# Kernel optimization log

Hardware: AMD Instinct MI355X
Metric: run time of the kernel (lower is better)

The kernel has to match this reference:

```python
import jax, jax.numpy as jnp
import numpy as np

EPS = 1e-12

def _l2norm(v, axis):
    return v / jnp.maximum(jnp.linalg.norm(v, axis=axis, keepdims=True), EPS)

def setup_inputs() -> dict:
    key = jax.random.key(0)
    k1, k2, k3 = jax.random.split(key, 3)
    B, D, C = 65536, 768, 100
    P = C * (C - 1) // 2  # 4950 pairwise local heads
    x = jax.random.normal(k1, (B, D), dtype=jnp.float32)
    first_out = jax.random.normal(k2, (B, C), dtype=jnp.float32)
    weights = jax.random.normal(k3, (P, 2, D), dtype=jnp.float32) * (1.0 / np.sqrt(D))
    sigma = jnp.ones((P,), dtype=jnp.float32)
    return {"x": x, "first_out": first_out, "weights": weights, "sigma": sigma, "cur_stage": 4}

def reference(x, first_out, weights, sigma, cur_stage):
    # top-2 class indices per sample, sorted ascending -> pair key (a, b), a < b
    _, top2 = jax.lax.top_k(first_out, 2)              # [B, 2]
    sorted_idx = jnp.sort(top2, axis=1)                # [B, 2]
    a = sorted_idx[:, 0]
    b = sorted_idx[:, 1]
    pair_idx = b * (b - 1) // 2 + a                    # key 'a-b' -> flat head index
    W = weights[pair_idx]                              # [B, 2, D] gathered expert weights
    s = sigma[pair_idx]                                # [B]
    # CosineLinear (use_RP=False): sigma * normalize(x) @ normalize(W)^T
    xn = _l2norm(x, axis=1)                            # [B, D]
    Wn = _l2norm(W, axis=2)                            # [B, 2, D]
    logits = s[:, None] * jnp.einsum('bd,bkd->bk', xn, Wn)  # [B, 2]
    # pick which of the two candidate classes the local head prefers
    sel = jnp.argmax(logits, axis=1)                   # [B]
    preds = jnp.take_along_axis(sorted_idx, sel[:, None], axis=1)[:, 0]  # [B]
    return preds, logits
```

## Files before the change

### kernel.cpp

```cpp
#include <hip/hip_runtime.h>
#include <math.h>


#define D_DIM 768
#define C_DIM 100
#define F4_PER_ROW (D_DIM / 4)
#define EPS_N 1e-12f

__device__ __forceinline__ bool vi_gt(float v0, int i0, float v1, int i1) {
    return (v0 > v1) || (v0 == v1 && i0 < i1);
}

__global__ __launch_bounds__(256) void mlcl_kernel(
    const float* __restrict__ x,
    const float* __restrict__ first_out,
    const float* __restrict__ weights,
    const float* __restrict__ sigma,
    float* __restrict__ out,
    int B)
{
    const int lane = threadIdx.x & 63;
    const int wave = threadIdx.x >> 6;
    const int r = blockIdx.x * 4 + wave;
    if (r >= B) return;

    const float* fo = first_out + (size_t)r * C_DIM;
    float e0 = fo[lane];
    int   j1 = lane + 64;
    float e1 = (j1 < C_DIM) ? fo[j1] : -INFINITY;

    float v1, v2; int i1, i2;
    if (vi_gt(e1, j1, e0, lane)) { v1 = e1; i1 = j1;  v2 = e0; i2 = lane; }
    else                         { v1 = e0; i1 = lane; v2 = e1; i2 = j1; }

    #pragma unroll
    for (int m = 1; m < 64; m <<= 1) {
        float ov1 = __shfl_xor(v1, m, 64);
        int   oi1 = __shfl_xor(i1, m, 64);
        float ov2 = __shfl_xor(v2, m, 64);
        int   oi2 = __shfl_xor(i2, m, 64);
        if (vi_gt(ov1, oi1, v1, i1)) {
            float nv2; int ni2;
            if (vi_gt(v1, i1, ov2, oi2)) { nv2 = v1;  ni2 = i1; }
            else                         { nv2 = ov2; ni2 = oi2; }
            v1 = ov1; i1 = oi1; v2 = nv2; i2 = ni2;
        } else {
            if (vi_gt(ov1, oi1, v2, i2)) { v2 = ov1; i2 = oi1; }
        }
    }
    const int a = min(i1, i2);
    const int b = max(i1, i2);
    const int pair = b * (b - 1) / 2 + a;

    const float4* xv = (const float4*)(x + (size_t)r * D_DIM);
    const float4* w0 = (const float4*)(weights + (size_t)pair * (2 * D_DIM));
    const float4* w1 = w0 + F4_PER_ROW;

    double xx = 0.0, d0 = 0.0, d1 = 0.0, n0 = 0.0, n1 = 0.0;
    #pragma unroll
    for (int j = 0; j < 3; ++j) {
        const int idx = lane + j * 64;
        float4 xa = xv[idx];
        float4 wa = w0[idx];
        float4 wb = w1[idx];
        xx += (double)xa.x * xa.x + (double)xa.y * xa.y + (double)xa.z * xa.z + (double)xa.w * xa.w;
        d0 += (double)xa.x * wa.x + (double)xa.y * wa.y + (double)xa.z * wa.z + (double)xa.w * wa.w;
        d1 += (double)xa.x * wb.x + (double)xa.y * wb.y + (double)xa.z * wb.z + (double)xa.w * wb.w;
        n0 += (double)wa.x * wa.x + (double)wa.y * wa.y + (double)wa.z * wa.z + (double)wa.w * wa.w;
        n1 += (double)wb.x * wb.x + (double)wb.y * wb.y + (double)wb.z * wb.z + (double)wb.w * wb.w;
    }
    #pragma unroll
    for (int m = 1; m < 64; m <<= 1) {
        xx += __shfl_xor(xx, m, 64);
        d0 += __shfl_xor(d0, m, 64);
        d1 += __shfl_xor(d1, m, 64);
        n0 += __shfl_xor(n0, m, 64);
        n1 += __shfl_xor(n1, m, 64);
    }

    if (lane == 0) {
        double s   = (double)sigma[pair];
        double inx = 1.0 / fmax(sqrt(xx), (double)EPS_N);
        double l0  = s * d0 * inx / fmax(sqrt(n0), (double)EPS_N);
        double l1  = s * d1 * inx / fmax(sqrt(n1), (double)EPS_N);
        int sel = (l1 > l0) ? 1 : 0;
        out[r] = (float)(sel ? b : a);
        out[B + 2 * r]     = (float)l0;
        out[B + 2 * r + 1] = (float)l1;
    }
}

extern "C" void kernel_launch(void* const* d_in, const int* in_sizes, int n_in,
                              void* d_out, int out_size, void* d_ws, size_t ws_size,
                              hipStream_t stream) {
    const float* x         = (const float*)d_in[0];
    const float* first_out = (const float*)d_in[1];
    const float* weights   = (const float*)d_in[2];
    const float* sigma     = (const float*)d_in[3];
    float* out = (float*)d_out;

    const int B = in_sizes[0] / D_DIM;
    dim3 grid((B + 3) / 4), block(256);
    hipLaunchKernelGGL(mlcl_kernel, grid, block, 0, stream,
                       x, first_out, weights, sigma, out, B);
}
```

Measured before the change: 336.0 us.

## Precompute per-head weight inverse norms and split top-2 into separate kernel

Adds a kernel that computes the inverse L2 norm of each of the 9900 weight rows once, instead of recomputing both norms for every sample. The top-2 selection moves into its own kernel that writes packed (a,b) indices to workspace, and the main kernel reads them. The x self-norm is accumulated in float instead of double, which cuts FP64 work but may introduce small rounding differences. The cost is two extra launches plus a workspace round trip for the indices.

```diff
diff --git a/kernel.cpp b/kernel.cpp
--- a/kernel.cpp
+++ b/kernel.cpp
@@ -4,24 +4,43 @@
 
 #define D_DIM 768
 #define C_DIM 100
+#define P_DIM 4950
 #define F4_PER_ROW (D_DIM / 4)
-#define EPS_N 1e-12f
+#define EPS_N 1e-12
 
 __device__ __forceinline__ bool vi_gt(float v0, int i0, float v1, int i1) {
     return (v0 > v1) || (v0 == v1 && i0 < i1);
 }
 
-__global__ __launch_bounds__(256) void mlcl_kernel(
-    const float* __restrict__ x,
+__global__ __launch_bounds__(256) void norm_kernel(
+    const float* __restrict__ weights,
+    double* __restrict__ invn,
+    int nrows)
+{
+    const int lane = threadIdx.x & 63;
+    const int row = (blockIdx.x << 2) + (threadIdx.x >> 6);
+    if (row >= nrows) return;
+
+    const float4* wv = (const float4*)(weights + (size_t)row * D_DIM);
+    double n = 0.0;
+    #pragma unroll
+    for (int j = 0; j < 3; ++j) {
+        float4 w = wv[lane + j * 64];
+        n += (double)w.x * w.x + (double)w.y * w.y
+           + (double)w.z * w.z + (double)w.w * w.w;
+    }
+    #pragma unroll
+    for (int m = 1; m < 64; m <<= 1) n += __shfl_xor(n, m, 64);
+    if (lane == 0) invn[row] = 1.0 / fmax(sqrt(n), EPS_N);
+}
+
+__global__ __launch_bounds__(256) void top2_kernel(
     const float* __restrict__ first_out,
-    const float* __restrict__ weights,
-    const float* __restrict__ sigma,
-    float* __restrict__ out,
+    int* __restrict__ abbuf,
     int B)
 {
     const int lane = threadIdx.x & 63;
-    const int wave = threadIdx.x >> 6;
-    const int r = blockIdx.x * 4 + wave;
+    const int r = (blockIdx.x << 2) + (threadIdx.x >> 6);
     if (r >= B) return;
 
     const float* fo = first_out + (size_t)r * C_DIM;
@@ -30,7 +49,7 @@
     float e1 = (j1 < C_DIM) ? fo[j1] : -INFINITY;
 
     float v1, v2; int i1, i2;
-    if (vi_gt(e1, j1, e0, lane)) { v1 = e1; i1 = j1;  v2 = e0; i2 = lane; }
+    if (vi_gt(e1, j1, e0, lane)) { v1 = e1; i1 = j1;   v2 = e0; i2 = lane; }
     else                         { v1 = e0; i1 = lane; v2 = e1; i2 = j1; }
 
     #pragma unroll
@@ -48,41 +67,61 @@
             if (vi_gt(ov1, oi1, v2, i2)) { v2 = ov1; i2 = oi1; }
         }
     }
-    const int a = min(i1, i2);
-    const int b = max(i1, i2);
+    if (lane == 0) {
+        const int a = min(i1, i2);
+        const int b = max(i1, i2);
+        abbuf[r] = a | (b << 16);
+    }
+}
+
+__global__ __launch_bounds__(256) void main_kernel(
+    const float* __restrict__ x,
+    const float* __restrict__ weights,
+    const float* __restrict__ sigma,
+    const double* __restrict__ invn,
+    const int* __restrict__ abbuf,
+    float* __restrict__ out,
+    int B)
+{
+    const int lane = threadIdx.x & 63;
+    const int r = (blockIdx.x << 2) + (threadIdx.x >> 6);
+    if (r >= B) return;
+
+    const int ab = abbuf[r];
+    const int a = ab & 0xffff;
+    const int b = ab >> 16;
     const int pair = b * (b - 1) / 2 + a;
 
     const float4* xv = (const float4*)(x + (size_t)r * D_DIM);
     const float4* w0 = (const float4*)(weights + (size_t)pair * (2 * D_DIM));
     const float4* w1 = w0 + F4_PER_ROW;
 
-    double xx = 0.0, d0 = 0.0, d1 = 0.0, n0 = 0.0, n1 = 0.0;
+    float  xx = 0.0f;
+    double d0 = 0.0, d1 = 0.0;
     #pragma unroll
     for (int j = 0; j < 3; ++j) {
         const int idx = lane + j * 64;
         float4 xa = xv[idx];
         float4 wa = w0[idx];
         float4 wb = w1[idx];
-        xx += (double)xa.x * xa.x + (double)xa.y * xa.y + (double)xa.z * xa.z + (double)xa.w * xa.w;
-        d0 += (double)xa.x * wa.x + (double)xa.y * wa.y + (double)xa.z * wa.z + (double)xa.w * wa.w;
-        d1 += (double)xa.x * wb.x + (double)xa.y * wb.y + (double)xa.z * wb.z + (double)xa.w * wb.w;
-        n0 += (double)wa.x * wa.x + (double)wa.y * wa.y + (double)wa.z * wa.z + (double)wa.w * wa.w;
-        n1 += (double)wb.x * wb.x + (double)wb.y * wb.y + (double)wb.z * wb.z + (double)wb.w * wb.w;
+        xx += xa.x * xa.x + xa.y * xa.y + xa.z * xa.z + xa.w * xa.w;
+        d0 += (double)xa.x * wa.x + (double)xa.y * wa.y
+            + (double)xa.z * wa.z + (double)xa.w * wa.w;
+        d1 += (double)xa.x * wb.x + (double)xa.y * wb.y
+            + (double)xa.z * wb.z + (double)xa.w * wb.w;
     }
     #pragma unroll
     for (int m = 1; m < 64; m <<= 1) {
         xx += __shfl_xor(xx, m, 64);
         d0 += __shfl_xor(d0, m, 64);
         d1 += __shfl_xor(d1, m, 64);
-        n0 += __shfl_xor(n0, m, 64);
-        n1 += __shfl_xor(n1, m, 64);
     }
 
     if (lane == 0) {
-        double s   = (double)sigma[pair];
-        double inx = 1.0 / fmax(sqrt(xx), (double)EPS_N);
-        double l0  = s * d0 * inx / fmax(sqrt(n0), (double)EPS_N);
-        double l1  = s * d1 * inx / fmax(sqrt(n1), (double)EPS_N);
+        double s    = (double)sigma[pair];
+        double sinx = s / fmax(sqrt((double)xx), EPS_N);
+        double l0   = sinx * d0 * invn[2 * pair];
+        double l1   = sinx * d1 * invn[2 * pair + 1];
         int sel = (l1 > l0) ? 1 : 0;
         out[r] = (float)(sel ? b : a);
         out[B + 2 * r]     = (float)l0;
@@ -100,7 +139,15 @@
     float* out = (float*)d_out;
 
     const int B = in_sizes[0] / D_DIM;
-    dim3 grid((B + 3) / 4), block(256);
-    hipLaunchKernelGGL(mlcl_kernel, grid, block, 0, stream,
-                       x, first_out, weights, sigma, out, B);
+    const int NW = 2 * P_DIM;
+
+    double* invn = (double*)d_ws;
+    int* abbuf   = (int*)((char*)d_ws + (size_t)NW * sizeof(double));
+
+    hipLaunchKernelGGL(norm_kernel, dim3((NW + 3) / 4), dim3(256), 0, stream,
+                       weights, invn, NW);
+    hipLaunchKernelGGL(top2_kernel, dim3((B + 3) / 4), dim3(256), 0, stream,
+                       first_out, abbuf, B);
+    hipLaunchKernelGGL(main_kernel, dim3((B + 3) / 4), dim3(256), 0, stream,
+                       x, weights, sigma, invn, abbuf, out, B);
 }
```

Result: no change. 335.7 us (-0.1%).

## Bucket rows by expert pair to reuse gathered weights and precomputed norms

Applied to the files above, without the earlier changes.

Splits the kernel into a top-2 pass that records pair ids and counts, a prefix scan, a scatter building per-pair row lists, and a per-pair kernel. Each pair block loads its two weight rows into registers once and computes their norms once, then processes the rows assigned to that pair, two at a time per wave. This removes the repeated per-row weight gathers and norm computations, at the cost of extra launches, atomics, a serial single-block scan and uneven work per block.

```diff
diff --git a/kernel.cpp b/kernel.cpp
--- a/kernel.cpp
+++ b/kernel.cpp
@@ -4,24 +4,29 @@
 
 #define D_DIM 768
 #define C_DIM 100
-#define F4_PER_ROW (D_DIM / 4)
-#define EPS_N 1e-12f
+#define P_DIM 4950
+#define F4_ROW (D_DIM / 4)
+#define EPS_N 1e-12
+
+typedef float vf4 __attribute__((ext_vector_type(4)));
 
 __device__ __forceinline__ bool vi_gt(float v0, int i0, float v1, int i1) {
     return (v0 > v1) || (v0 == v1 && i0 < i1);
 }
 
-__global__ __launch_bounds__(256) void mlcl_kernel(
-    const float* __restrict__ x,
+#define DOT4D(acc, u, v) \
+    acc += (double)u.x * v.x + (double)u.y * v.y + (double)u.z * v.z + (double)u.w * v.w
+#define SQ4F(acc, u) \
+    acc += u.x * u.x + u.y * u.y + u.z * u.z + u.w * u.w
+
+__global__ __launch_bounds__(256) void top2_kernel(
     const float* __restrict__ first_out,
-    const float* __restrict__ weights,
-    const float* __restrict__ sigma,
-    float* __restrict__ out,
+    int* __restrict__ pairbuf,
+    int* __restrict__ counts,
     int B)
 {
     const int lane = threadIdx.x & 63;
-    const int wave = threadIdx.x >> 6;
-    const int r = blockIdx.x * 4 + wave;
+    const int r = (blockIdx.x << 2) + (threadIdx.x >> 6);
     if (r >= B) return;
 
     const float* fo = first_out + (size_t)r * C_DIM;
@@ -30,7 +35,7 @@
     float e1 = (j1 < C_DIM) ? fo[j1] : -INFINITY;
 
     float v1, v2; int i1, i2;
-    if (vi_gt(e1, j1, e0, lane)) { v1 = e1; i1 = j1;  v2 = e0; i2 = lane; }
+    if (vi_gt(e1, j1, e0, lane)) { v1 = e1; i1 = j1;   v2 = e0; i2 = lane; }
     else                         { v1 = e0; i1 = lane; v2 = e1; i2 = j1; }
 
     #pragma unroll
@@ -48,45 +53,147 @@
             if (vi_gt(ov1, oi1, v2, i2)) { v2 = ov1; i2 = oi1; }
         }
     }
-    const int a = min(i1, i2);
-    const int b = max(i1, i2);
-    const int pair = b * (b - 1) / 2 + a;
-
-    const float4* xv = (const float4*)(x + (size_t)r * D_DIM);
-    const float4* w0 = (const float4*)(weights + (size_t)pair * (2 * D_DIM));
-    const float4* w1 = w0 + F4_PER_ROW;
-
-    double xx = 0.0, d0 = 0.0, d1 = 0.0, n0 = 0.0, n1 = 0.0;
+    if (lane == 0) {
+        const int a = min(i1, i2);
+        const int b = max(i1, i2);
+        const int p = b * (b - 1) / 2 + a;
+        pairbuf[r] = p;
+        atomicAdd(&counts[p], 1);
+    }
+}
+
+#define SCAN_T 256
+#define CHUNK ((P_DIM + SCAN_T - 1) / SCAN_T)
+__global__ __launch_bounds__(SCAN_T) void scan_kernel(
+    const int* __restrict__ counts,
+    int* __restrict__ offsets)
+{
+    __shared__ int sh[SCAN_T];
+    const int t = threadIdx.x;
+    int vals[CHUNK];
+    int tot = 0;
+    #pragma unroll
+    for (int j = 0; j < CHUNK; ++j) {
+        const int idx = t * CHUNK + j;
+        const int v = (idx < P_DIM) ? counts[idx] : 0;
+        vals[j] = v; tot += v;
+    }
+    sh[t] = tot;
+    __syncthreads();
+    for (int d = 1; d < SCAN_T; d <<= 1) {
+        const int v = (t >= d) ? sh[t - d] : 0;
+        __syncthreads();
+        sh[t] += v;
+        __syncthreads();
+    }
+    int run = (t == 0) ? 0 : sh[t - 1];
+    #pragma unroll
+    for (int j = 0; j < CHUNK; ++j) {
+        const int idx = t * CHUNK + j;
+        if (idx < P_DIM) offsets[idx] = run;
+        run += vals[j];
+    }
+}
+
+__global__ __launch_bounds__(256) void scatter_kernel(
+    const int* __restrict__ pairbuf,
+    const int* __restrict__ offsets,
+    int* __restrict__ cursors,
+    int* __restrict__ rowlist,
+    int B)
+{
+    const int r = blockIdx.x * 256 + threadIdx.x;
+    if (r >= B) return;
+    const int p = pairbuf[r];
+    const int pos = offsets[p] + atomicAdd(&cursors[p], 1);
+    rowlist[pos] = r;
+}
+
+__global__ __launch_bounds__(256) void pair_kernel(
+    const float* __restrict__ x,
+    const float* __restrict__ weights,
+    const float* __restrict__ sigma,
+    const int* __restrict__ counts,
+    const int* __restrict__ offsets,
+    const int* __restrict__ rowlist,
+    float* __restrict__ out,
+    int B)
+{
+    const int p = blockIdx.x;
+    const int cnt = counts[p];
+    if (cnt == 0) return;
+    const int base = offsets[p];
+    const int lane = threadIdx.x & 63;
+    const int wave = threadIdx.x >> 6;
+
+    int b = (int)floor((sqrt(8.0 * (double)p + 1.0) + 1.0) * 0.5);
+    if (b * (b - 1) / 2 > p) --b;
+    if ((b + 1) * b / 2 <= p) ++b;
+    const int a = p - b * (b - 1) / 2;
+
+    const vf4* wv = (const vf4*)(weights + (size_t)p * (2 * D_DIM));
+    vf4 w0[3], w1[3];
+    double n0 = 0.0, n1 = 0.0;
     #pragma unroll
     for (int j = 0; j < 3; ++j) {
-        const int idx = lane + j * 64;
-        float4 xa = xv[idx];
-        float4 wa = w0[idx];
-        float4 wb = w1[idx];
-        xx += (double)xa.x * xa.x + (double)xa.y * xa.y + (double)xa.z * xa.z + (double)xa.w * xa.w;
-        d0 += (double)xa.x * wa.x + (double)xa.y * wa.y + (double)xa.z * wa.z + (double)xa.w * wa.w;
-        d1 += (double)xa.x * wb.x + (double)xa.y * wb.y + (double)xa.z * wb.z + (double)xa.w * wb.w;
-        n0 += (double)wa.x * wa.x + (double)wa.y * wa.y + (double)wa.z * wa.z + (double)wa.w * wa.w;
-        n1 += (double)wb.x * wb.x + (double)wb.y * wb.y + (double)wb.z * wb.z + (double)wb.w * wb.w;
+        w0[j] = wv[lane + j * 64];
+        w1[j] = wv[F4_ROW + lane + j * 64];
+        DOT4D(n0, w0[j], w0[j]);
+        DOT4D(n1, w1[j], w1[j]);
     }
     #pragma unroll
     for (int m = 1; m < 64; m <<= 1) {
-        xx += __shfl_xor(xx, m, 64);
-        d0 += __shfl_xor(d0, m, 64);
-        d1 += __shfl_xor(d1, m, 64);
         n0 += __shfl_xor(n0, m, 64);
         n1 += __shfl_xor(n1, m, 64);
     }
-
-    if (lane == 0) {
-        double s   = (double)sigma[pair];
-        double inx = 1.0 / fmax(sqrt(xx), (double)EPS_N);
-        double l0  = s * d0 * inx / fmax(sqrt(n0), (double)EPS_N);
-        double l1  = s * d1 * inx / fmax(sqrt(n1), (double)EPS_N);
-        int sel = (l1 > l0) ? 1 : 0;
-        out[r] = (float)(sel ? b : a);
-        out[B + 2 * r]     = (float)l0;
-        out[B + 2 * r + 1] = (float)l1;
+    const double s    = (double)sigma[p];
+    const double si0  = s / fmax(sqrt(n0), EPS_N);
+    const double si1  = s / fmax(sqrt(n1), EPS_N);
+
+    for (int i = wave * 2; i < cnt; i += 8) {
+        const int r0 = rowlist[base + i];
+        const bool has2 = (i + 1 < cnt);
+        const int r1 = has2 ? rowlist[base + i + 1] : r0;
+
+        const vf4* xa = (const vf4*)(x + (size_t)r0 * D_DIM);
+        const vf4* xb = (const vf4*)(x + (size_t)r1 * D_DIM);
+
+        float  xx0 = 0.f, xx1 = 0.f;
+        double d00 = 0.0, d01 = 0.0, d10 = 0.0, d11 = 0.0;
+        #pragma unroll
+        for (int j = 0; j < 3; ++j) {
+            const vf4 va = xa[lane + j * 64];
+            const vf4 vb = xb[lane + j * 64];
+            SQ4F(xx0, va);
+            SQ4F(xx1, vb);
+            DOT4D(d00, va, w0[j]);
+            DOT4D(d01, va, w1[j]);
+            DOT4D(d10, vb, w0[j]);
+            DOT4D(d11, vb, w1[j]);
+        }
+        #pragma unroll
+        for (int m = 1; m < 64; m <<= 1) {
+            xx0 += __shfl_xor(xx0, m, 64);
+            xx1 += __shfl_xor(xx1, m, 64);
+            d00 += __shfl_xor(d00, m, 64);
+            d01 += __shfl_xor(d01, m, 64);
+            d10 += __shfl_xor(d10, m, 64);
+            d11 += __shfl_xor(d11, m, 64);
+        }
+
+        if (lane == 0 || (lane == 1 && has2)) {
+            const int    rr  = lane ? r1 : r0;
+            const float  xxv = lane ? xx1 : xx0;
+            const double dd0 = lane ? d10 : d00;
+            const double dd1 = lane ? d11 : d01;
+            const double inx = 1.0 / fmax(sqrt((double)xxv), EPS_N);
+            const double l0  = si0 * dd0 * inx;
+            const double l1  = si1 * dd1 * inx;
+            const int sel = (l1 > l0) ? 1 : 0;
+            out[rr] = (float)(sel ? b : a);
+            out[B + 2 * rr]     = (float)l0;
+            out[B + 2 * rr + 1] = (float)l1;
+        }
     }
 }
 
@@ -100,7 +207,21 @@
     float* out = (float*)d_out;
 
     const int B = in_sizes[0] / D_DIM;
-    dim3 grid((B + 3) / 4), block(256);
-    hipLaunchKernelGGL(mlcl_kernel, grid, block, 0, stream,
-                       x, first_out, weights, sigma, out, B);
-}
+    const int P = in_sizes[3];
+
+    int* counts  = (int*)d_ws;
+    int* cursors = counts + P;
+    int* offsets = cursors + P;
+    int* pairbuf = offsets + P;
+    int* rowlist = pairbuf + B;
+
+    hipMemsetAsync(counts, 0, 2 * (size_t)P * sizeof(int), stream);
+    hipLaunchKernelGGL(top2_kernel, dim3((B + 3) / 4), dim3(256), 0, stream,
+                       first_out, pairbuf, counts, B);
+    hipLaunchKernelGGL(scan_kernel, dim3(1), dim3(SCAN_T), 0, stream,
+                       counts, offsets);
+    hipLaunchKernelGGL(scatter_kernel, dim3((B + 255) / 256), dim3(256), 0, stream,
+                       pairbuf, offsets, cursors, rowlist, B);
+    hipLaunchKernelGGL(pair_kernel, dim3(P), dim3(256), 0, stream,
+                       x, weights, sigma, counts, offsets, rowlist, out, B);
+}
```

Result: slower. 363.9 us (+8.3%).

## Assign four threads per row instead of a full wavefront per row

Applied to the files above, without the earlier changes.

Each output row is now handled by a group of 4 lanes rather than a whole 64-lane wavefront. Every lane runs a serial top-2 scan over its slice of first_out and accumulates the dot products over 48 float4 steps, so the cross-lane shuffle reductions shrink from 6 stages to 2. The x squared-norm accumulator also drops from double to float, and the two logits are written with a single float2 store. The intent is to cut shuffle and reduction overhead and the idle lanes, at the cost of strided, less coalesced float4 loads per lane and a longer serial loop per thread.

```diff
diff --git a/kernel.cpp b/kernel.cpp
--- a/kernel.cpp
+++ b/kernel.cpp
@@ -4,14 +4,21 @@
 
 #define D_DIM 768
 #define C_DIM 100
-#define F4_PER_ROW (D_DIM / 4)
-#define EPS_N 1e-12f
+#define EPS_N 1e-12
+
+typedef float vf4 __attribute__((ext_vector_type(4)));
 
 __device__ __forceinline__ bool vi_gt(float v0, int i0, float v1, int i1) {
     return (v0 > v1) || (v0 == v1 && i0 < i1);
 }
 
-__global__ __launch_bounds__(256) void mlcl_kernel(
+__device__ __forceinline__ void t2up(float val, int idx,
+                                     float& v1, int& i1, float& v2, int& i2) {
+    if (vi_gt(val, idx, v1, i1)) { v2 = v1; i2 = i1; v1 = val; i1 = idx; }
+    else if (vi_gt(val, idx, v2, i2)) { v2 = val; i2 = idx; }
+}
+
+__global__ __launch_bounds__(256) void fused_kernel(
     const float* __restrict__ x,
     const float* __restrict__ first_out,
     const float* __restrict__ weights,
@@ -19,22 +26,28 @@
     float* __restrict__ out,
     int B)
 {
-    const int lane = threadIdx.x & 63;
-    const int wave = threadIdx.x >> 6;
-    const int r = blockIdx.x * 4 + wave;
+    const int tid = blockIdx.x * 256 + threadIdx.x;
+    const int gl  = tid & 3;
+    const int r   = tid >> 2;
     if (r >= B) return;
 
-    const float* fo = first_out + (size_t)r * C_DIM;
-    float e0 = fo[lane];
-    int   j1 = lane + 64;
-    float e1 = (j1 < C_DIM) ? fo[j1] : -INFINITY;
-
-    float v1, v2; int i1, i2;
-    if (vi_gt(e1, j1, e0, lane)) { v1 = e1; i1 = j1;  v2 = e0; i2 = lane; }
-    else                         { v1 = e0; i1 = lane; v2 = e1; i2 = j1; }
-
+    const vf4* fov = (const vf4*)(first_out + (size_t)r * C_DIM);
+    float v1 = -INFINITY, v2 = -INFINITY;
+    int   i1 = 0x7fffffff, i2 = 0x7fffffff;
     #pragma unroll
-    for (int m = 1; m < 64; m <<= 1) {
+    for (int t = 0; t < 7; ++t) {
+        const int f4i = 4 * t + gl;
+        if (f4i < 25) {
+            vf4 e = fov[f4i];
+            const int e0 = 4 * f4i;
+            t2up(e.x, e0,     v1, i1, v2, i2);
+            t2up(e.y, e0 + 1, v1, i1, v2, i2);
+            t2up(e.z, e0 + 2, v1, i1, v2, i2);
+            t2up(e.w, e0 + 3, v1, i1, v2, i2);
+        }
+    }
+    #pragma unroll
+    for (int m = 1; m < 4; m <<= 1) {
         float ov1 = __shfl_xor(v1, m, 64);
         int   oi1 = __shfl_xor(i1, m, 64);
         float ov2 = __shfl_xor(v2, m, 64);
@@ -50,27 +63,31 @@
     }
     const int a = min(i1, i2);
     const int b = max(i1, i2);
-    const int pair = b * (b - 1) / 2 + a;
+    const int p = b * (b - 1) / 2 + a;
 
-    const float4* xv = (const float4*)(x + (size_t)r * D_DIM);
-    const float4* w0 = (const float4*)(weights + (size_t)pair * (2 * D_DIM));
-    const float4* w1 = w0 + F4_PER_ROW;
+    const vf4* xv = (const vf4*)(x + (size_t)r * D_DIM);
+    const vf4* wv = (const vf4*)(weights + (size_t)p * (2 * D_DIM));
 
-    double xx = 0.0, d0 = 0.0, d1 = 0.0, n0 = 0.0, n1 = 0.0;
-    #pragma unroll
-    for (int j = 0; j < 3; ++j) {
-        const int idx = lane + j * 64;
-        float4 xa = xv[idx];
-        float4 wa = w0[idx];
-        float4 wb = w1[idx];
-        xx += (double)xa.x * xa.x + (double)xa.y * xa.y + (double)xa.z * xa.z + (double)xa.w * xa.w;
-        d0 += (double)xa.x * wa.x + (double)xa.y * wa.y + (double)xa.z * wa.z + (double)xa.w * wa.w;
-        d1 += (double)xa.x * wb.x + (double)xa.y * wb.y + (double)xa.z * wb.z + (double)xa.w * wb.w;
-        n0 += (double)wa.x * wa.x + (double)wa.y * wa.y + (double)wa.z * wa.z + (double)wa.w * wa.w;
-        n1 += (double)wb.x * wb.x + (double)wb.y * wb.y + (double)wb.z * wb.z + (double)wb.w * wb.w;
+    float  xx = 0.f;
+    double d0 = 0.0, d1 = 0.0, n0 = 0.0, n1 = 0.0;
+    #pragma unroll 4
+    for (int tt = 0; tt < 48; ++tt) {
+        const int f4i = 4 * tt + gl;
+        vf4 xa = xv[f4i];
+        vf4 w0 = wv[f4i];
+        vf4 w1 = wv[192 + f4i];
+        xx += xa.x * xa.x + xa.y * xa.y + xa.z * xa.z + xa.w * xa.w;
+        d0 += (double)xa.x * w0.x + (double)xa.y * w0.y
+            + (double)xa.z * w0.z + (double)xa.w * w0.w;
+        d1 += (double)xa.x * w1.x + (double)xa.y * w1.y
+            + (double)xa.z * w1.z + (double)xa.w * w1.w;
+        n0 += (double)w0.x * w0.x + (double)w0.y * w0.y
+            + (double)w0.z * w0.z + (double)w0.w * w0.w;
+        n1 += (double)w1.x * w1.x + (double)w1.y * w1.y
+            + (double)w1.z * w1.z + (double)w1.w * w1.w;
     }
     #pragma unroll
-    for (int m = 1; m < 64; m <<= 1) {
+    for (int m = 1; m < 4; m <<= 1) {
         xx += __shfl_xor(xx, m, 64);
         d0 += __shfl_xor(d0, m, 64);
         d1 += __shfl_xor(d1, m, 64);
@@ -78,15 +95,15 @@
         n1 += __shfl_xor(n1, m, 64);
     }
 
-    if (lane == 0) {
-        double s   = (double)sigma[pair];
-        double inx = 1.0 / fmax(sqrt(xx), (double)EPS_N);
-        double l0  = s * d0 * inx / fmax(sqrt(n0), (double)EPS_N);
-        double l1  = s * d1 * inx / fmax(sqrt(n1), (double)EPS_N);
-        int sel = (l1 > l0) ? 1 : 0;
+    if (gl == 0) {
+        const double s   = (double)sigma[p];
+        const double inx = s / fmax(sqrt((double)xx), EPS_N);
+        const double l0  = inx * d0 / fmax(sqrt(n0), EPS_N);
+        const double l1  = inx * d1 / fmax(sqrt(n1), EPS_N);
+        const int sel = (l1 > l0) ? 1 : 0;
         out[r] = (float)(sel ? b : a);
-        out[B + 2 * r]     = (float)l0;
-        out[B + 2 * r + 1] = (float)l1;
+        float2 lg = make_float2((float)l0, (float)l1);
+        *(float2*)(out + B + 2 * (size_t)r) = lg;
     }
 }
 
@@ -100,7 +117,7 @@
     float* out = (float*)d_out;
 
     const int B = in_sizes[0] / D_DIM;
-    dim3 grid((B + 3) / 4), block(256);
-    hipLaunchKernelGGL(mlcl_kernel, grid, block, 0, stream,
-                       x, first_out, weights, sigma, out, B);
+    const int threads = B * 4;
+    hipLaunchKernelGGL(fused_kernel, dim3((threads + 255) / 256), dim3(256),
+                       0, stream, x, first_out, weights, sigma, out, B);
 }
```

Measured after the change: 368.7 us. 1.1x slower.
